# Kernel optimization log

Measured on AMD Instinct MI355X. Metric: run time of the kernel, lower is better.

The kernel has to match this reference:

```python
import jax, jax.numpy as jnp
import numpy as np
from jax import lax

B, H, W, C_IN, C_OUT = 32, 56, 56, 256, 256
KH, KW = 3, 3

def setup_inputs() -> dict:
    key = jax.random.key(0)
    k_in, k_kern, k_bias = jax.random.split(key, 3)
    inputs = jax.random.normal(k_in, (B, H, W, C_IN), dtype=jnp.float32)
    # lecun_normal (flax default_kernel_init): std = 1/sqrt(fan_in)
    fan_in = KH * KW * C_IN
    kernel = jax.random.normal(k_kern, (KH, KW, C_IN, C_OUT), dtype=jnp.float32) / jnp.sqrt(fan_in).astype(jnp.float32)
    bias = jnp.zeros((C_OUT,), dtype=jnp.float32)
    return {"inputs": inputs, "kernel": kernel, "bias": bias}

def reference(inputs, kernel, bias):
    # QuantConv forward with config noise == 0.0: plain NHWC/HWIO conv + bias.
    y = lax.conv_general_dilated(
        inputs, kernel,
        window_strides=(1, 1),
        padding='SAME',
        lhs_dilation=(1, 1),
        rhs_dilation=(1, 1),
        dimension_numbers=('NHWC', 'HWIO', 'NHWC'),
        feature_group_count=1,
    )
    return y + bias
```

## Files before the change

### kernel.cpp

```cpp
#include <hip/hip_runtime.h>
#include <hip/hip_bf16.h>
#include <stdint.h>


#define IMG_B 32
#define IMG_H 56
#define IMG_W 56
#define CIN   256
#define COUT  256
#define KDIM  2304
#define M_TOT 100352
#define HW    (IMG_H * IMG_W)
#define PW    58
#define PHW   (PW * PW)
#define BK    64
#define ITERS (KDIM / BK)

typedef __bf16 bf16_t;
typedef bf16_t bf16x8 __attribute__((ext_vector_type(8)));
typedef float  f32x4  __attribute__((ext_vector_type(4)));
typedef float  f32x16 __attribute__((ext_vector_type(16)));

typedef const __attribute__((address_space(1))) void GV;
typedef __attribute__((address_space(3))) void LV;

__device__ __forceinline__ void async16(const bf16_t* g, bf16_t* l) {
    __builtin_amdgcn_global_load_lds((GV*)g, (LV*)l, 16, 0, 0);
}

__global__ void prep_pad(const float* __restrict__ in, bf16_t* __restrict__ out) {
    const size_t e = ((size_t)blockIdx.x * 256 + threadIdx.x) * 8;
    const int pix = (int)(e >> 8);
    const int c0  = (int)(e & 255);
    const int b   = pix / PHW;
    const int r   = pix - b * PHW;
    const int py  = r / PW;
    const int px  = r - py * PW;
    bf16x8 v = {};
    if (py >= 1 && py <= IMG_H && px >= 1 && px <= IMG_W) {
        const f32x4* s = (const f32x4*)(in +
            ((((size_t)b * IMG_H + (py - 1)) * IMG_W + (px - 1)) << 8) + c0);
        f32x4 a = s[0], bq = s[1];
        #pragma unroll
        for (int k = 0; k < 4; ++k) v[k] = (bf16_t)a[k];
        #pragma unroll
        for (int k = 0; k < 4; ++k) v[4 + k] = (bf16_t)bq[k];
    }
    *(bf16x8*)(out + e) = v;
}

__global__ void prep_weights(const float* __restrict__ kern, bf16_t* __restrict__ wt) {
    int idx = blockIdx.x * 256 + threadIdx.x;
    int co  = idx / KDIM;
    int k   = idx - co * KDIM;
    wt[idx] = (bf16_t)kern[k * COUT + co];
}

__global__ __launch_bounds__(256)
void conv_mfma_p(const bf16_t* __restrict__ P, const bf16_t* __restrict__ wt,
                 const float* __restrict__ bias, float* __restrict__ out)
{
    __shared__ bf16_t Al[128 * BK];
    __shared__ bf16_t Bl[128 * BK];

    const int tid  = threadIdx.x;
    const int wave = tid >> 6;
    const int lane = tid & 63;

    const int bid   = blockIdx.x;
    const int tile  = (bid & 7) * 196 + (bid >> 3);
    const int ntile = tile & 1;
    const int mtile = tile >> 1;

    const int rl = lane >> 3;
    const int sl = lane & 7;
    const int u  = sl ^ rl;

    const bf16_t* asrc[4];
    const bf16_t* bsrc[4];
    bf16_t* alds[4];
    bf16_t* blds[4];
    #pragma unroll
    for (int i = 0; i < 4; ++i) {
        const int row = wave * 32 + i * 8 + rl;
        const int m   = mtile * 128 + row;
        const int bb  = m / HW;
        const int rem = m - bb * HW;
        const int yy  = rem / IMG_W;
        const int xx  = rem - yy * IMG_W;
        asrc[i] = P + (((size_t)bb * PHW + yy * PW + xx) << 8) + u * 8;
        const int co = ntile * 128 + row;
        bsrc[i] = wt + (size_t)co * KDIM + u * 8;
        alds[i] = &Al[(wave * 32 + i * 8) * BK];
        blds[i] = &Bl[(wave * 32 + i * 8) * BK];
    }

    const int wm = wave & 1;
    const int wn = wave >> 1;
    const int ln = lane & 31;
    const int lh = lane >> 5;
    const int rx = ln & 7;

    f32x16 acc[2][2] = {};

    #pragma unroll
    for (int i = 0; i < 4; ++i) {
        async16(asrc[i], alds[i]);
        async16(bsrc[i], blds[i]);
    }

    #pragma unroll 1
    for (int it = 0; it < ITERS; ++it) {
        __syncthreads();

        bf16x8 af[2][4], bf[2][4];
        #pragma unroll
        for (int kk = 0; kk < 4; ++kk) {
            const int slot = ((kk * 2 + lh) ^ rx) * 8;
            #pragma unroll
            for (int g = 0; g < 2; ++g) {
                af[g][kk] = *(const bf16x8*)(&Al[(wm * 64 + g * 32 + ln) * BK + slot]);
                bf[g][kk] = *(const bf16x8*)(&Bl[(wn * 64 + g * 32 + ln) * BK + slot]);
            }
        }

        __syncthreads();

        if (it + 1 < ITERS) {
            const int itn  = it + 1;
            const int tap  = itn >> 2;
            const int kh   = tap / 3;
            const int kw   = tap - kh * 3;
            const int koff = ((kh * PW + kw) << 8) + ((itn & 3) << 6);
            const int woff = itn * BK;
            #pragma unroll
            for (int i = 0; i < 4; ++i) {
                async16(asrc[i] + koff, alds[i]);
                async16(bsrc[i] + woff, blds[i]);
            }
        }

        #pragma unroll
        for (int kk = 0; kk < 4; ++kk)
            #pragma unroll
            for (int g = 0; g < 2; ++g)
                #pragma unroll
                for (int h = 0; h < 2; ++h)
                    acc[g][h] = __builtin_amdgcn_mfma_f32_32x32x16_bf16(
                        af[g][kk], bf[h][kk], acc[g][h], 0, 0, 0);
    }

    const int mbase  = mtile * 128 + wm * 64;
    const int cobase = ntile * 128 + wn * 64;
    float bv[2];
    #pragma unroll
    for (int h = 0; h < 2; ++h) bv[h] = bias[cobase + h * 32 + ln];

    #pragma unroll
    for (int g = 0; g < 2; ++g) {
        #pragma unroll
        for (int reg = 0; reg < 16; ++reg) {
            const int mm = mbase + g * 32 + (reg & 3) + 8 * (reg >> 2) + 4 * lh;
            float* op = out + (size_t)mm * COUT + cobase + ln;
            op[0]  = acc[g][0][reg] + bv[0];
            op[32] = acc[g][1][reg] + bv[1];
        }
    }
}

#define ASTR 40
#define BSTR 40
__global__ __launch_bounds__(256)
void conv_mfma(const float* __restrict__ in, const bf16_t* __restrict__ wt,
               const float* __restrict__ bias, float* __restrict__ out)
{
    __shared__ bf16_t Alf[128 * ASTR];
    __shared__ bf16_t Blf[128 * BSTR];

    const int tid   = threadIdx.x;
    const int ntile = blockIdx.x & 1;
    const int mtile = blockIdx.x >> 1;

    const int arow = tid >> 1;
    const int aseg = tid & 1;
    const int m    = mtile * 128 + arow;
    const int bb   = m / HW;
    const int rem  = m - bb * HW;
    const int yy   = rem / IMG_W;
    const int xx   = rem - yy * IMG_W;

    const bf16_t* wt_row = wt + (size_t)(ntile * 128 + arow) * KDIM + aseg * 16;

    const int wave = tid >> 6;
    const int lane = tid & 63;
    const int wm   = wave & 1;
    const int wn   = wave >> 1;
    const int lrow = lane & 15;
    const int q    = lane >> 4;

    f32x4 acc[4][4] = {};

    #pragma unroll 1
    for (int it = 0; it < 72; ++it) {
        const int tap = it >> 3;
        const int kh  = tap / 3;
        const int kw  = tap - kh * 3;
        const int ci0 = (it & 7) << 5;

        const int iy = yy + kh - 1;
        const int ix = xx + kw - 1;
        const bool valid = ((unsigned)iy < IMG_H) && ((unsigned)ix < IMG_W);

        f32x4 va[4] = {};
        if (valid) {
            const f32x4* src = (const f32x4*)(in +
                ((((size_t)bb * IMG_H + iy) * IMG_W + ix) * CIN + ci0 + aseg * 16));
            va[0] = src[0]; va[1] = src[1]; va[2] = src[2]; va[3] = src[3];
        }
        const uint4 wb0 = *(const uint4*)(wt_row + it * 32);
        const uint4 wb1 = *(const uint4*)(wt_row + it * 32 + 8);

        __syncthreads();

        bf16x8 pa0, pa1;
        #pragma unroll
        for (int e = 0; e < 8; ++e) pa0[e] = (bf16_t)va[e >> 2][e & 3];
        #pragma unroll
        for (int e = 0; e < 8; ++e) pa1[e] = (bf16_t)va[2 + (e >> 2)][e & 3];
        *(bf16x8*)(&Alf[arow * ASTR + aseg * 16])     = pa0;
        *(bf16x8*)(&Alf[arow * ASTR + aseg * 16 + 8]) = pa1;
        *(uint4*)(&Blf[arow * BSTR + aseg * 16])      = wb0;
        *(uint4*)(&Blf[arow * BSTR + aseg * 16 + 8])  = wb1;

        __syncthreads();

        bf16x8 af[4], bf[4];
        #pragma unroll
        for (int i = 0; i < 4; ++i)
            af[i] = *(const bf16x8*)(&Alf[(wm * 64 + i * 16 + lrow) * ASTR + q * 8]);
        #pragma unroll
        for (int j = 0; j < 4; ++j)
            bf[j] = *(const bf16x8*)(&Blf[(wn * 64 + j * 16 + lrow) * BSTR + q * 8]);

        #pragma unroll
        for (int i = 0; i < 4; ++i)
            #pragma unroll
            for (int j = 0; j < 4; ++j)
                acc[i][j] = __builtin_amdgcn_mfma_f32_16x16x32_bf16(af[i], bf[j], acc[i][j], 0, 0, 0);
    }

    const int co_base = ntile * 128 + wn * 64;
    float bv[4];
    #pragma unroll
    for (int j = 0; j < 4; ++j) bv[j] = bias[co_base + j * 16 + lrow];

    const int mrow_base = mtile * 128 + wm * 64;
    #pragma unroll
    for (int i = 0; i < 4; ++i) {
        #pragma unroll
        for (int rr = 0; rr < 4; ++rr) {
            const int mm = mrow_base + i * 16 + q * 4 + rr;
            float* op = out + (size_t)mm * COUT + co_base;
            #pragma unroll
            for (int j = 0; j < 4; ++j)
                op[j * 16 + lrow] = acc[i][j][rr] + bv[j];
        }
    }
}

extern "C" void kernel_launch(void* const* d_in, const int* in_sizes, int n_in,
                              void* d_out, int out_size, void* d_ws, size_t ws_size,
                              hipStream_t stream) {
    const float* inputs = (const float*)d_in[0];
    const float* kernel = (const float*)d_in[1];
    const float* bias   = (const float*)d_in[2];
    float*       outp   = (float*)d_out;

    const size_t p_elems = (size_t)IMG_B * PHW * CIN;
    const size_t p_bytes = p_elems * sizeof(bf16_t);
    const size_t w_bytes = (size_t)KDIM * COUT * sizeof(bf16_t);

    if (ws_size >= p_bytes + w_bytes) {
        bf16_t* pimg = (bf16_t*)d_ws;
        bf16_t* wt   = (bf16_t*)((char*)d_ws + p_bytes);
        prep_pad<<<(int)(p_elems / 8 / 256), 256, 0, stream>>>(inputs, pimg);
        prep_weights<<<KDIM * COUT / 256, 256, 0, stream>>>(kernel, wt);
        conv_mfma_p<<<(M_TOT / 128) * 2, 256, 0, stream>>>(pimg, wt, bias, outp);
    } else {
        bf16_t* wt = (bf16_t*)d_ws;
        prep_weights<<<KDIM * COUT / 256, 256, 0, stream>>>(kernel, wt);
        conv_mfma<<<(M_TOT / 128) * 2, 256, 0, stream>>>(inputs, wt, bias, outp);
    }
}
```

Measured before the change: 312.7 us.

## Fuse pad and weight prep kernels; use fragment-ordered LDS layout for MFMA

Merges the input pad/convert and weight transpose kernels into a single launch, removing one kernel launch and its gap. The LDS tile layout changes from XOR-swizzled rows to a fragment-major layout: each lane's 16-byte chunk is placed contiguously, so MFMA operand reads become linear lane*16B loads with constant offsets and address arithmetic drops. Each global_load_lds now fetches 16-byte pieces with a 32-byte stride per row (two lanes per row per call), which may reduce global load coalescing compared with the previous full 128-byte row segments.

```diff
diff --git a/kernel.cpp b/kernel.cpp
--- a/kernel.cpp
+++ b/kernel.cpp
@@ -15,6 +15,8 @@
 #define PHW   (PW * PW)
 #define BK    64
 #define ITERS (KDIM / BK)
+#define PAD_BLOCKS 13456
+#define WT_BLOCKS  (KDIM * COUT / 256)
 
 typedef __bf16 bf16_t;
 typedef bf16_t bf16x8 __attribute__((ext_vector_type(8)));
@@ -28,25 +30,33 @@
     __builtin_amdgcn_global_load_lds((GV*)g, (LV*)l, 16, 0, 0);
 }
 
-__global__ void prep_pad(const float* __restrict__ in, bf16_t* __restrict__ out) {
-    const size_t e = ((size_t)blockIdx.x * 256 + threadIdx.x) * 8;
-    const int pix = (int)(e >> 8);
-    const int c0  = (int)(e & 255);
-    const int b   = pix / PHW;
-    const int r   = pix - b * PHW;
-    const int py  = r / PW;
-    const int px  = r - py * PW;
-    bf16x8 v = {};
-    if (py >= 1 && py <= IMG_H && px >= 1 && px <= IMG_W) {
-        const f32x4* s = (const f32x4*)(in +
-            ((((size_t)b * IMG_H + (py - 1)) * IMG_W + (px - 1)) << 8) + c0);
-        f32x4 a = s[0], bq = s[1];
-        #pragma unroll
-        for (int k = 0; k < 4; ++k) v[k] = (bf16_t)a[k];
-        #pragma unroll
-        for (int k = 0; k < 4; ++k) v[4 + k] = (bf16_t)bq[k];
-    }
-    *(bf16x8*)(out + e) = v;
+__global__ void prep_fused(const float* __restrict__ in, const float* __restrict__ kern,
+                           bf16_t* __restrict__ pimg, bf16_t* __restrict__ wt) {
+    if (blockIdx.x < PAD_BLOCKS) {
+        const size_t e = ((size_t)blockIdx.x * 256 + threadIdx.x) * 8;
+        const int pix = (int)(e >> 8);
+        const int c0  = (int)(e & 255);
+        const int b   = pix / PHW;
+        const int r   = pix - b * PHW;
+        const int py  = r / PW;
+        const int px  = r - py * PW;
+        bf16x8 v = {};
+        if (py >= 1 && py <= IMG_H && px >= 1 && px <= IMG_W) {
+            const f32x4* s = (const f32x4*)(in +
+                ((((size_t)b * IMG_H + (py - 1)) * IMG_W + (px - 1)) << 8) + c0);
+            f32x4 a = s[0], bq = s[1];
+            #pragma unroll
+            for (int k = 0; k < 4; ++k) v[k] = (bf16_t)a[k];
+            #pragma unroll
+            for (int k = 0; k < 4; ++k) v[4 + k] = (bf16_t)bq[k];
+        }
+        *(bf16x8*)(pimg + e) = v;
+    } else {
+        const int idx = (blockIdx.x - PAD_BLOCKS) * 256 + threadIdx.x;
+        const int co  = idx / KDIM;
+        const int k   = idx - co * KDIM;
+        wt[idx] = (bf16_t)kern[k * COUT + co];
+    }
 }
 
 __global__ void prep_weights(const float* __restrict__ kern, bf16_t* __restrict__ wt) {
@@ -60,8 +70,8 @@
 void conv_mfma_p(const bf16_t* __restrict__ P, const bf16_t* __restrict__ wt,
                  const float* __restrict__ bias, float* __restrict__ out)
 {
-    __shared__ bf16_t Al[128 * BK];
-    __shared__ bf16_t Bl[128 * BK];
+    __shared__ __align__(1024) bf16_t Al[128 * BK];
+    __shared__ __align__(1024) bf16_t Bl[128 * BK];
 
     const int tid  = threadIdx.x;
     const int wave = tid >> 6;
@@ -72,42 +82,30 @@
     const int ntile = tile & 1;
     const int mtile = tile >> 1;
 
-    const int rl = lane >> 3;
-    const int sl = lane & 7;
-    const int u  = sl ^ rl;
-
-    const bf16_t* asrc[4];
-    const bf16_t* bsrc[4];
-    bf16_t* alds[4];
-    bf16_t* blds[4];
-    #pragma unroll
-    for (int i = 0; i < 4; ++i) {
-        const int row = wave * 32 + i * 8 + rl;
-        const int m   = mtile * 128 + row;
-        const int bb  = m / HW;
-        const int rem = m - bb * HW;
-        const int yy  = rem / IMG_W;
-        const int xx  = rem - yy * IMG_W;
-        asrc[i] = P + (((size_t)bb * PHW + yy * PW + xx) << 8) + u * 8;
-        const int co = ntile * 128 + row;
-        bsrc[i] = wt + (size_t)co * KDIM + u * 8;
-        alds[i] = &Al[(wave * 32 + i * 8) * BK];
-        blds[i] = &Bl[(wave * 32 + i * 8) * BK];
-    }
+    const int ln32 = lane & 31;
+    const int lh   = lane >> 5;
+    const int arow = wave * 32 + ln32;
+    const int m    = mtile * 128 + arow;
+    const int bb   = m / HW;
+    const int rem  = m - bb * HW;
+    const int yy   = rem / IMG_W;
+    const int xx   = rem - yy * IMG_W;
+    const bf16_t* asrc = P + (((size_t)bb * PHW + yy * PW + xx) << 8) + lh * 8;
+    const bf16_t* bsrc = wt + (size_t)(ntile * 128 + arow) * KDIM + lh * 8;
+    bf16_t* alds = &Al[wave * 2048];
+    bf16_t* blds = &Bl[wave * 2048];
 
     const int wm = wave & 1;
     const int wn = wave >> 1;
-    const int ln = lane & 31;
-    const int lh = lane >> 5;
-    const int rx = ln & 7;
+    const bf16_t* rA = Al + wm * 4096 + lane * 8;
+    const bf16_t* rB = Bl + wn * 4096 + lane * 8;
 
     f32x16 acc[2][2] = {};
 
     #pragma unroll
-    for (int i = 0; i < 4; ++i) {
-        async16(asrc[i], alds[i]);
-        async16(bsrc[i], blds[i]);
-    }
+    for (int kk = 0; kk < 4; ++kk) async16(asrc + kk * 16, alds + kk * 512);
+    #pragma unroll
+    for (int kk = 0; kk < 4; ++kk) async16(bsrc + kk * 16, blds + kk * 512);
 
     #pragma unroll 1
     for (int it = 0; it < ITERS; ++it) {
@@ -116,12 +114,10 @@
         bf16x8 af[2][4], bf[2][4];
         #pragma unroll
         for (int kk = 0; kk < 4; ++kk) {
-            const int slot = ((kk * 2 + lh) ^ rx) * 8;
-            #pragma unroll
-            for (int g = 0; g < 2; ++g) {
-                af[g][kk] = *(const bf16x8*)(&Al[(wm * 64 + g * 32 + ln) * BK + slot]);
-                bf[g][kk] = *(const bf16x8*)(&Bl[(wn * 64 + g * 32 + ln) * BK + slot]);
-            }
+            af[0][kk] = *(const bf16x8*)(rA + kk * 512);
+            af[1][kk] = *(const bf16x8*)(rA + 2048 + kk * 512);
+            bf[0][kk] = *(const bf16x8*)(rB + kk * 512);
+            bf[1][kk] = *(const bf16x8*)(rB + 2048 + kk * 512);
         }
 
         __syncthreads();
@@ -134,33 +130,33 @@
             const int koff = ((kh * PW + kw) << 8) + ((itn & 3) << 6);
             const int woff = itn * BK;
             #pragma unroll
-            for (int i = 0; i < 4; ++i) {
-                async16(asrc[i] + koff, alds[i]);
-                async16(bsrc[i] + woff, blds[i]);
-            }
-        }
-
-        #pragma unroll
-        for (int kk = 0; kk < 4; ++kk)
-            #pragma unroll
-            for (int g = 0; g < 2; ++g)
-                #pragma unroll
-                for (int h = 0; h < 2; ++h)
-                    acc[g][h] = __builtin_amdgcn_mfma_f32_32x32x16_bf16(
-                        af[g][kk], bf[h][kk], acc[g][h], 0, 0, 0);
-    }
-
+            for (int kk = 0; kk < 4; ++kk) async16(asrc + koff + kk * 16, alds + kk * 512);
+            #pragma unroll
+            for (int kk = 0; kk < 4; ++kk) async16(bsrc + woff + kk * 16, blds + kk * 512);
+        }
+
+        #pragma unroll
+        for (int kk = 0; kk < 4; ++kk) {
+            acc[0][0] = __builtin_amdgcn_mfma_f32_32x32x16_bf16(af[0][kk], bf[0][kk], acc[0][0], 0, 0, 0);
+            acc[0][1] = __builtin_amdgcn_mfma_f32_32x32x16_bf16(af[0][kk], bf[1][kk], acc[0][1], 0, 0, 0);
+            acc[1][0] = __builtin_amdgcn_mfma_f32_32x32x16_bf16(af[1][kk], bf[0][kk], acc[1][0], 0, 0, 0);
+            acc[1][1] = __builtin_amdgcn_mfma_f32_32x32x16_bf16(af[1][kk], bf[1][kk], acc[1][1], 0, 0, 0);
+        }
+    }
+
+    const int ln     = lane & 31;
+    const int lhh    = lane >> 5;
     const int mbase  = mtile * 128 + wm * 64;
     const int cobase = ntile * 128 + wn * 64;
     float bv[2];
-    #pragma unroll
-    for (int h = 0; h < 2; ++h) bv[h] = bias[cobase + h * 32 + ln];
+    bv[0] = bias[cobase + ln];
+    bv[1] = bias[cobase + 32 + ln];
 
     #pragma unroll
     for (int g = 0; g < 2; ++g) {
         #pragma unroll
         for (int reg = 0; reg < 16; ++reg) {
-            const int mm = mbase + g * 32 + (reg & 3) + 8 * (reg >> 2) + 4 * lh;
+            const int mm = mbase + g * 32 + (reg & 3) + 8 * (reg >> 2) + 4 * lhh;
             float* op = out + (size_t)mm * COUT + cobase + ln;
             op[0]  = acc[g][0][reg] + bv[0];
             op[32] = acc[g][1][reg] + bv[1];
@@ -283,12 +279,11 @@
     if (ws_size >= p_bytes + w_bytes) {
         bf16_t* pimg = (bf16_t*)d_ws;
         bf16_t* wt   = (bf16_t*)((char*)d_ws + p_bytes);
-        prep_pad<<<(int)(p_elems / 8 / 256), 256, 0, stream>>>(inputs, pimg);
-        prep_weights<<<KDIM * COUT / 256, 256, 0, stream>>>(kernel, wt);
+        prep_fused<<<PAD_BLOCKS + WT_BLOCKS, 256, 0, stream>>>(inputs, kernel, pimg, wt);
         conv_mfma_p<<<(M_TOT / 128) * 2, 256, 0, stream>>>(pimg, wt, bias, outp);
     } else {
         bf16_t* wt = (bf16_t*)d_ws;
-        prep_weights<<<KDIM * COUT / 256, 256, 0, stream>>>(kernel, wt);
+        prep_weights<<<WT_BLOCKS, 256, 0, stream>>>(kernel, wt);
         conv_mfma<<<(M_TOT / 128) * 2, 256, 0, stream>>>(inputs, wt, bias, outp);
     }
 }
```

After: 413.6 us. +32.3%, slower.

## Double-buffer LDS tiles with two-stage async prefetch and fuse prep kernels

Applied to the files above, without the earlier changes.

The conv main loop moves from a single LDS buffer to two. Tiles are prefetched two iterations ahead, with explicit vmcnt waits and raw barriers so global-to-LDS loads overlap the MFMA work, and MFMA sections run at raised wave priority. The padding and weight-transpose prep kernels are merged into one launch to save a kernel launch. LDS use doubles to 64KB per block, which may lower occupancy, and the hand-written waitcnt counts depend on the exact number of loads issued.

```diff
diff --git a/kernel.cpp b/kernel.cpp
--- a/kernel.cpp
+++ b/kernel.cpp
@@ -15,6 +15,9 @@
 #define PHW   (PW * PW)
 #define BK    64
 #define ITERS (KDIM / BK)
+#define TILE_E (128 * BK)
+#define PAD_BLOCKS 13456
+#define WT_BLOCKS  (KDIM * COUT / 256)
 
 typedef __bf16 bf16_t;
 typedef bf16_t bf16x8 __attribute__((ext_vector_type(8)));
@@ -28,25 +31,33 @@
     __builtin_amdgcn_global_load_lds((GV*)g, (LV*)l, 16, 0, 0);
 }
 
-__global__ void prep_pad(const float* __restrict__ in, bf16_t* __restrict__ out) {
-    const size_t e = ((size_t)blockIdx.x * 256 + threadIdx.x) * 8;
-    const int pix = (int)(e >> 8);
-    const int c0  = (int)(e & 255);
-    const int b   = pix / PHW;
-    const int r   = pix - b * PHW;
-    const int py  = r / PW;
-    const int px  = r - py * PW;
-    bf16x8 v = {};
-    if (py >= 1 && py <= IMG_H && px >= 1 && px <= IMG_W) {
-        const f32x4* s = (const f32x4*)(in +
-            ((((size_t)b * IMG_H + (py - 1)) * IMG_W + (px - 1)) << 8) + c0);
-        f32x4 a = s[0], bq = s[1];
-        #pragma unroll
-        for (int k = 0; k < 4; ++k) v[k] = (bf16_t)a[k];
-        #pragma unroll
-        for (int k = 0; k < 4; ++k) v[4 + k] = (bf16_t)bq[k];
-    }
-    *(bf16x8*)(out + e) = v;
+__global__ void prep_fused(const float* __restrict__ in, const float* __restrict__ kern,
+                           bf16_t* __restrict__ pimg, bf16_t* __restrict__ wt) {
+    if (blockIdx.x < PAD_BLOCKS) {
+        const size_t e = ((size_t)blockIdx.x * 256 + threadIdx.x) * 8;
+        const int pix = (int)(e >> 8);
+        const int c0  = (int)(e & 255);
+        const int b   = pix / PHW;
+        const int r   = pix - b * PHW;
+        const int py  = r / PW;
+        const int px  = r - py * PW;
+        bf16x8 v = {};
+        if (py >= 1 && py <= IMG_H && px >= 1 && px <= IMG_W) {
+            const f32x4* s = (const f32x4*)(in +
+                ((((size_t)b * IMG_H + (py - 1)) * IMG_W + (px - 1)) << 8) + c0);
+            f32x4 a = s[0], bq = s[1];
+            #pragma unroll
+            for (int k = 0; k < 4; ++k) v[k] = (bf16_t)a[k];
+            #pragma unroll
+            for (int k = 0; k < 4; ++k) v[4 + k] = (bf16_t)bq[k];
+        }
+        *(bf16x8*)(pimg + e) = v;
+    } else {
+        const int idx = (blockIdx.x - PAD_BLOCKS) * 256 + threadIdx.x;
+        const int co  = idx / KDIM;
+        const int k   = idx - co * KDIM;
+        wt[idx] = (bf16_t)kern[k * COUT + co];
+    }
 }
 
 __global__ void prep_weights(const float* __restrict__ kern, bf16_t* __restrict__ wt) {
@@ -56,12 +67,55 @@
     wt[idx] = (bf16_t)kern[k * COUT + co];
 }
 
+
+#define STAGE(t1, cb) do { \
+    const int tap_  = (t1) >> 2; \
+    const int kh_   = tap_ / 3; \
+    const int kw_   = tap_ - kh_ * 3; \
+    const int koff_ = ((kh_ * PW + kw_) << 8) + (((t1) & 3) << 6); \
+    const int woff_ = (t1) * BK; \
+    _Pragma("unroll") \
+    for (int i_ = 0; i_ < 4; ++i_) { \
+        async16(asrc[i_] + koff_, alds[i_] + (cb) * TILE_E); \
+        async16(bsrc[i_] + woff_, blds[i_] + (cb) * TILE_E); \
+    } \
+} while (0)
+
+#define STEP(t, cur) do { \
+    if ((t) + 1 < ITERS) asm volatile("s_waitcnt vmcnt(8)" ::: "memory"); \
+    else                 asm volatile("s_waitcnt vmcnt(0)" ::: "memory"); \
+    __builtin_amdgcn_s_barrier(); \
+    __builtin_amdgcn_sched_barrier(0); \
+    bf16x8 af[2][4], bfr[2][4]; \
+    _Pragma("unroll") \
+    for (int kk = 0; kk < 4; ++kk) { \
+        const int slot_ = ((kk * 2 + lh) ^ rx) * 8; \
+        af[0][kk]  = *(const bf16x8*)(&Al[cur][(wm * 64 + ln) * BK + slot_]); \
+        af[1][kk]  = *(const bf16x8*)(&Al[cur][(wm * 64 + 32 + ln) * BK + slot_]); \
+        bfr[0][kk] = *(const bf16x8*)(&Bl[cur][(wn * 64 + ln) * BK + slot_]); \
+        bfr[1][kk] = *(const bf16x8*)(&Bl[cur][(wn * 64 + 32 + ln) * BK + slot_]); \
+    } \
+    asm volatile("s_waitcnt lgkmcnt(0)" ::: "memory"); \
+    __builtin_amdgcn_s_barrier(); \
+    __builtin_amdgcn_sched_barrier(0); \
+    if ((t) + 2 < ITERS) STAGE((t) + 2, cur); \
+    __builtin_amdgcn_s_setprio(1); \
+    _Pragma("unroll") \
+    for (int kk = 0; kk < 4; ++kk) { \
+        acc[0][0] = __builtin_amdgcn_mfma_f32_32x32x16_bf16(af[0][kk], bfr[0][kk], acc[0][0], 0, 0, 0); \
+        acc[0][1] = __builtin_amdgcn_mfma_f32_32x32x16_bf16(af[0][kk], bfr[1][kk], acc[0][1], 0, 0, 0); \
+        acc[1][0] = __builtin_amdgcn_mfma_f32_32x32x16_bf16(af[1][kk], bfr[0][kk], acc[1][0], 0, 0, 0); \
+        acc[1][1] = __builtin_amdgcn_mfma_f32_32x32x16_bf16(af[1][kk], bfr[1][kk], acc[1][1], 0, 0, 0); \
+    } \
+    __builtin_amdgcn_s_setprio(0); \
+} while (0)
+
 __global__ __launch_bounds__(256)
 void conv_mfma_p(const bf16_t* __restrict__ P, const bf16_t* __restrict__ wt,
                  const float* __restrict__ bias, float* __restrict__ out)
 {
-    __shared__ bf16_t Al[128 * BK];
-    __shared__ bf16_t Bl[128 * BK];
+    __shared__ bf16_t Al[2][TILE_E];
+    __shared__ bf16_t Bl[2][TILE_E];
 
     const int tid  = threadIdx.x;
     const int wave = tid >> 6;
@@ -91,8 +145,8 @@
         asrc[i] = P + (((size_t)bb * PHW + yy * PW + xx) << 8) + u * 8;
         const int co = ntile * 128 + row;
         bsrc[i] = wt + (size_t)co * KDIM + u * 8;
-        alds[i] = &Al[(wave * 32 + i * 8) * BK];
-        blds[i] = &Bl[(wave * 32 + i * 8) * BK];
+        alds[i] = &Al[0][(wave * 32 + i * 8) * BK];
+        blds[i] = &Bl[0][(wave * 32 + i * 8) * BK];
     }
 
     const int wm = wave & 1;
@@ -103,58 +157,21 @@
 
     f32x16 acc[2][2] = {};
 
-    #pragma unroll
-    for (int i = 0; i < 4; ++i) {
-        async16(asrc[i], alds[i]);
-        async16(bsrc[i], blds[i]);
-    }
+    STAGE(0, 0);
+    STAGE(1, 1);
 
     #pragma unroll 1
-    for (int it = 0; it < ITERS; ++it) {
-        __syncthreads();
-
-        bf16x8 af[2][4], bf[2][4];
-        #pragma unroll
-        for (int kk = 0; kk < 4; ++kk) {
-            const int slot = ((kk * 2 + lh) ^ rx) * 8;
-            #pragma unroll
-            for (int g = 0; g < 2; ++g) {
-                af[g][kk] = *(const bf16x8*)(&Al[(wm * 64 + g * 32 + ln) * BK + slot]);
-                bf[g][kk] = *(const bf16x8*)(&Bl[(wn * 64 + g * 32 + ln) * BK + slot]);
-            }
-        }
-
-        __syncthreads();
-
-        if (it + 1 < ITERS) {
-            const int itn  = it + 1;
-            const int tap  = itn >> 2;
-            const int kh   = tap / 3;
-            const int kw   = tap - kh * 3;
-            const int koff = ((kh * PW + kw) << 8) + ((itn & 3) << 6);
-            const int woff = itn * BK;
-            #pragma unroll
-            for (int i = 0; i < 4; ++i) {
-                async16(asrc[i] + koff, alds[i]);
-                async16(bsrc[i] + woff, blds[i]);
-            }
-        }
-
-        #pragma unroll
-        for (int kk = 0; kk < 4; ++kk)
-            #pragma unroll
-            for (int g = 0; g < 2; ++g)
-                #pragma unroll
-                for (int h = 0; h < 2; ++h)
-                    acc[g][h] = __builtin_amdgcn_mfma_f32_32x32x16_bf16(
-                        af[g][kk], bf[h][kk], acc[g][h], 0, 0, 0);
+    for (int it2 = 0; it2 < ITERS / 2; ++it2) {
+        const int t0 = it2 * 2;
+        STEP(t0,     0);
+        STEP(t0 + 1, 1);
     }
 
     const int mbase  = mtile * 128 + wm * 64;
     const int cobase = ntile * 128 + wn * 64;
     float bv[2];
-    #pragma unroll
-    for (int h = 0; h < 2; ++h) bv[h] = bias[cobase + h * 32 + ln];
+    bv[0] = bias[cobase + ln];
+    bv[1] = bias[cobase + 32 + ln];
 
     #pragma unroll
     for (int g = 0; g < 2; ++g) {
@@ -283,12 +300,11 @@
     if (ws_size >= p_bytes + w_bytes) {
         bf16_t* pimg = (bf16_t*)d_ws;
         bf16_t* wt   = (bf16_t*)((char*)d_ws + p_bytes);
-        prep_pad<<<(int)(p_elems / 8 / 256), 256, 0, stream>>>(inputs, pimg);
-        prep_weights<<<KDIM * COUT / 256, 256, 0, stream>>>(kernel, wt);
+        prep_fused<<<PAD_BLOCKS + WT_BLOCKS, 256, 0, stream>>>(inputs, kernel, pimg, wt);
         conv_mfma_p<<<(M_TOT / 128) * 2, 256, 0, stream>>>(pimg, wt, bias, outp);
     } else {
         bf16_t* wt = (bf16_t*)d_ws;
-        prep_weights<<<KDIM * COUT / 256, 256, 0, stream>>>(kernel, wt);
+        prep_weights<<<WT_BLOCKS, 256, 0, stream>>>(kernel, wt);
         conv_mfma<<<(M_TOT / 128) * 2, 256, 0, stream>>>(inputs, wt, bias, outp);
     }
 }
```

Result: slower. 321.4 us (+2.8%).

## Widen conv tile to full Cout with double-buffered B and fuse prep kernels

Applied to the files above, without the earlier changes.

The main convolution kernel now computes a 128x256 output tile per block instead of 128x128. Each A tile is therefore loaded once rather than twice, and the grid is halved. The weight tile gets double-buffered LDS (64 KB) and MFMA issue priority is raised with s_setprio. The pad and weight-transpose prep kernels are merged into one launch to save a launch. The trade-offs are more accumulator registers and LDS per block, which may cut occupancy below the two blocks per CU requested by the launch bounds. Only 784 blocks are launched across the CUs.

```diff
diff --git a/kernel.cpp b/kernel.cpp
--- a/kernel.cpp
+++ b/kernel.cpp
@@ -15,6 +15,8 @@
 #define PHW   (PW * PW)
 #define BK    64
 #define ITERS (KDIM / BK)
+#define PAD_BLOCKS 13456
+#define WT_BLOCKS  (KDIM * COUT / 256)
 
 typedef __bf16 bf16_t;
 typedef bf16_t bf16x8 __attribute__((ext_vector_type(8)));
@@ -28,25 +30,33 @@
     __builtin_amdgcn_global_load_lds((GV*)g, (LV*)l, 16, 0, 0);
 }
 
-__global__ void prep_pad(const float* __restrict__ in, bf16_t* __restrict__ out) {
-    const size_t e = ((size_t)blockIdx.x * 256 + threadIdx.x) * 8;
-    const int pix = (int)(e >> 8);
-    const int c0  = (int)(e & 255);
-    const int b   = pix / PHW;
-    const int r   = pix - b * PHW;
-    const int py  = r / PW;
-    const int px  = r - py * PW;
-    bf16x8 v = {};
-    if (py >= 1 && py <= IMG_H && px >= 1 && px <= IMG_W) {
-        const f32x4* s = (const f32x4*)(in +
-            ((((size_t)b * IMG_H + (py - 1)) * IMG_W + (px - 1)) << 8) + c0);
-        f32x4 a = s[0], bq = s[1];
-        #pragma unroll
-        for (int k = 0; k < 4; ++k) v[k] = (bf16_t)a[k];
-        #pragma unroll
-        for (int k = 0; k < 4; ++k) v[4 + k] = (bf16_t)bq[k];
-    }
-    *(bf16x8*)(out + e) = v;
+__global__ void prep_fused(const float* __restrict__ in, const float* __restrict__ kern,
+                           bf16_t* __restrict__ pimg, bf16_t* __restrict__ wt) {
+    if (blockIdx.x < PAD_BLOCKS) {
+        const size_t e = ((size_t)blockIdx.x * 256 + threadIdx.x) * 8;
+        const int pix = (int)(e >> 8);
+        const int c0  = (int)(e & 255);
+        const int b   = pix / PHW;
+        const int r   = pix - b * PHW;
+        const int py  = r / PW;
+        const int px  = r - py * PW;
+        bf16x8 v = {};
+        if (py >= 1 && py <= IMG_H && px >= 1 && px <= IMG_W) {
+            const f32x4* s = (const f32x4*)(in +
+                ((((size_t)b * IMG_H + (py - 1)) * IMG_W + (px - 1)) << 8) + c0);
+            f32x4 a = s[0], bq = s[1];
+            #pragma unroll
+            for (int k = 0; k < 4; ++k) v[k] = (bf16_t)a[k];
+            #pragma unroll
+            for (int k = 0; k < 4; ++k) v[4 + k] = (bf16_t)bq[k];
+        }
+        *(bf16x8*)(pimg + e) = v;
+    } else {
+        const int idx = (blockIdx.x - PAD_BLOCKS) * 256 + threadIdx.x;
+        const int co  = idx / KDIM;
+        const int k   = idx - co * KDIM;
+        wt[idx] = (bf16_t)kern[k * COUT + co];
+    }
 }
 
 __global__ void prep_weights(const float* __restrict__ kern, bf16_t* __restrict__ wt) {
@@ -56,30 +66,45 @@
     wt[idx] = (bf16_t)kern[k * COUT + co];
 }
 
-__global__ __launch_bounds__(256)
-void conv_mfma_p(const bf16_t* __restrict__ P, const bf16_t* __restrict__ wt,
-                 const float* __restrict__ bias, float* __restrict__ out)
+
+#define STAGE_A(t1) do { \
+    const int tap_  = (t1) >> 2; \
+    const int kh_   = tap_ / 3; \
+    const int kw_   = tap_ - kh_ * 3; \
+    const int koff_ = ((kh_ * PW + kw_) << 8) + (((t1) & 3) << 6); \
+    _Pragma("unroll") \
+    for (int i_ = 0; i_ < 4; ++i_) \
+        async16(asrc[i_] + koff_, alds[i_]); \
+} while (0)
+
+#define STAGE_B(t1, nb) do { \
+    const int woff_ = (t1) * BK; \
+    _Pragma("unroll") \
+    for (int i_ = 0; i_ < 8; ++i_) \
+        async16(bsrc0 + (size_t)i_ * (8 * KDIM) + woff_, \
+                &Bl[(nb)][(wave * 64 + i_ * 8) * BK]); \
+} while (0)
+
+__global__ __launch_bounds__(256, 2)
+void conv_wide(const bf16_t* __restrict__ P, const bf16_t* __restrict__ wt,
+               const float* __restrict__ bias, float* __restrict__ out)
 {
     __shared__ bf16_t Al[128 * BK];
-    __shared__ bf16_t Bl[128 * BK];
+    __shared__ bf16_t Bl[2][256 * BK];
 
     const int tid  = threadIdx.x;
     const int wave = tid >> 6;
     const int lane = tid & 63;
 
     const int bid   = blockIdx.x;
-    const int tile  = (bid & 7) * 196 + (bid >> 3);
-    const int ntile = tile & 1;
-    const int mtile = tile >> 1;
+    const int mtile = (bid & 7) * 98 + (bid >> 3);
 
     const int rl = lane >> 3;
     const int sl = lane & 7;
     const int u  = sl ^ rl;
 
     const bf16_t* asrc[4];
-    const bf16_t* bsrc[4];
     bf16_t* alds[4];
-    bf16_t* blds[4];
     #pragma unroll
     for (int i = 0; i < 4; ++i) {
         const int row = wave * 32 + i * 8 + rl;
@@ -89,11 +114,9 @@
         const int yy  = rem / IMG_W;
         const int xx  = rem - yy * IMG_W;
         asrc[i] = P + (((size_t)bb * PHW + yy * PW + xx) << 8) + u * 8;
-        const int co = ntile * 128 + row;
-        bsrc[i] = wt + (size_t)co * KDIM + u * 8;
         alds[i] = &Al[(wave * 32 + i * 8) * BK];
-        blds[i] = &Bl[(wave * 32 + i * 8) * BK];
-    }
+    }
+    const bf16_t* bsrc0 = wt + (size_t)(wave * 64 + rl) * KDIM + u * 8;
 
     const int wm = wave & 1;
     const int wn = wave >> 1;
@@ -101,60 +124,56 @@
     const int lh = lane >> 5;
     const int rx = ln & 7;
 
-    f32x16 acc[2][2] = {};
-
-    #pragma unroll
-    for (int i = 0; i < 4; ++i) {
-        async16(asrc[i], alds[i]);
-        async16(bsrc[i], blds[i]);
-    }
+    f32x16 acc[2][4] = {};
+
+    STAGE_A(0);
+    STAGE_B(0, 0);
 
     #pragma unroll 1
     for (int it = 0; it < ITERS; ++it) {
+        const int bc = it & 1;
         __syncthreads();
 
-        bf16x8 af[2][4], bf[2][4];
+        bf16x8 af[2][4];
         #pragma unroll
         for (int kk = 0; kk < 4; ++kk) {
             const int slot = ((kk * 2 + lh) ^ rx) * 8;
-            #pragma unroll
-            for (int g = 0; g < 2; ++g) {
-                af[g][kk] = *(const bf16x8*)(&Al[(wm * 64 + g * 32 + ln) * BK + slot]);
-                bf[g][kk] = *(const bf16x8*)(&Bl[(wn * 64 + g * 32 + ln) * BK + slot]);
-            }
+            af[0][kk] = *(const bf16x8*)(&Al[(wm * 64 + ln) * BK + slot]);
+            af[1][kk] = *(const bf16x8*)(&Al[(wm * 64 + 32 + ln) * BK + slot]);
         }
 
         __syncthreads();
 
         if (it + 1 < ITERS) {
-            const int itn  = it + 1;
-            const int tap  = itn >> 2;
-            const int kh   = tap / 3;
-            const int kw   = tap - kh * 3;
-            const int koff = ((kh * PW + kw) << 8) + ((itn & 3) << 6);
-            const int woff = itn * BK;
-            #pragma unroll
-            for (int i = 0; i < 4; ++i) {
-                async16(asrc[i] + koff, alds[i]);
-                async16(bsrc[i] + woff, blds[i]);
-            }
-        }
-
-        #pragma unroll
-        for (int kk = 0; kk < 4; ++kk)
-            #pragma unroll
-            for (int g = 0; g < 2; ++g)
-                #pragma unroll
-                for (int h = 0; h < 2; ++h)
-                    acc[g][h] = __builtin_amdgcn_mfma_f32_32x32x16_bf16(
-                        af[g][kk], bf[h][kk], acc[g][h], 0, 0, 0);
+            STAGE_A(it + 1);
+            STAGE_B(it + 1, bc ^ 1);
+        }
+
+        #pragma unroll
+        for (int kk = 0; kk < 4; ++kk) {
+            const int slot = ((kk * 2 + lh) ^ rx) * 8;
+            const bf16x8 bf0 = *(const bf16x8*)(&Bl[bc][(wn * 128 + ln) * BK + slot]);
+            const bf16x8 bf1 = *(const bf16x8*)(&Bl[bc][(wn * 128 + 32 + ln) * BK + slot]);
+            const bf16x8 bf2 = *(const bf16x8*)(&Bl[bc][(wn * 128 + 64 + ln) * BK + slot]);
+            const bf16x8 bf3 = *(const bf16x8*)(&Bl[bc][(wn * 128 + 96 + ln) * BK + slot]);
+            __builtin_amdgcn_s_setprio(1);
+            acc[0][0] = __builtin_amdgcn_mfma_f32_32x32x16_bf16(af[0][kk], bf0, acc[0][0], 0, 0, 0);
+            acc[0][1] = __builtin_amdgcn_mfma_f32_32x32x16_bf16(af[0][kk], bf1, acc[0][1], 0, 0, 0);
+            acc[0][2] = __builtin_amdgcn_mfma_f32_32x32x16_bf16(af[0][kk], bf2, acc[0][2], 0, 0, 0);
+            acc[0][3] = __builtin_amdgcn_mfma_f32_32x32x16_bf16(af[0][kk], bf3, acc[0][3], 0, 0, 0);
+            acc[1][0] = __builtin_amdgcn_mfma_f32_32x32x16_bf16(af[1][kk], bf0, acc[1][0], 0, 0, 0);
+            acc[1][1] = __builtin_amdgcn_mfma_f32_32x32x16_bf16(af[1][kk], bf1, acc[1][1], 0, 0, 0);
+            acc[1][2] = __builtin_amdgcn_mfma_f32_32x32x16_bf16(af[1][kk], bf2, acc[1][2], 0, 0, 0);
+            acc[1][3] = __builtin_amdgcn_mfma_f32_32x32x16_bf16(af[1][kk], bf3, acc[1][3], 0, 0, 0);
+            __builtin_amdgcn_s_setprio(0);
+        }
     }
 
     const int mbase  = mtile * 128 + wm * 64;
-    const int cobase = ntile * 128 + wn * 64;
-    float bv[2];
-    #pragma unroll
-    for (int h = 0; h < 2; ++h) bv[h] = bias[cobase + h * 32 + ln];
+    const int cobase = wn * 128;
+    float bv[4];
+    #pragma unroll
+    for (int j = 0; j < 4; ++j) bv[j] = bias[cobase + j * 32 + ln];
 
     #pragma unroll
     for (int g = 0; g < 2; ++g) {
@@ -162,8 +181,9 @@
         for (int reg = 0; reg < 16; ++reg) {
             const int mm = mbase + g * 32 + (reg & 3) + 8 * (reg >> 2) + 4 * lh;
             float* op = out + (size_t)mm * COUT + cobase + ln;
-            op[0]  = acc[g][0][reg] + bv[0];
-            op[32] = acc[g][1][reg] + bv[1];
+            #pragma unroll
+            for (int j = 0; j < 4; ++j)
+                op[j * 32] = acc[g][j][reg] + bv[j];
         }
     }
 }
@@ -283,12 +303,11 @@
     if (ws_size >= p_bytes + w_bytes) {
         bf16_t* pimg = (bf16_t*)d_ws;
         bf16_t* wt   = (bf16_t*)((char*)d_ws + p_bytes);
-        prep_pad<<<(int)(p_elems / 8 / 256), 256, 0, stream>>>(inputs, pimg);
-        prep_weights<<<KDIM * COUT / 256, 256, 0, stream>>>(kernel, wt);
-        conv_mfma_p<<<(M_TOT / 128) * 2, 256, 0, stream>>>(pimg, wt, bias, outp);
+        prep_fused<<<PAD_BLOCKS + WT_BLOCKS, 256, 0, stream>>>(inputs, kernel, pimg, wt);
+        conv_wide<<<M_TOT / 128, 256, 0, stream>>>(pimg, wt, bias, outp);
     } else {
         bf16_t* wt = (bf16_t*)d_ws;
-        prep_weights<<<KDIM * COUT / 256, 256, 0, stream>>>(kernel, wt);
+        prep_weights<<<WT_BLOCKS, 256, 0, stream>>>(kernel, wt);
         conv_mfma<<<(M_TOT / 128) * 2, 256, 0, stream>>>(inputs, wt, bias, outp);
     }
 }
```

After: 325.8 us. 4.2% more time.
